# Kernel tuning notes

Measured on AMD Instinct MI355X. Metric: run time of the kernel, lower is better.

## Reference

```python
import jax, jax.numpy as jnp
import numpy as np

N, E = 100000, 1600000
F_IN, H, C = 64, 64, 40


def setup_inputs() -> dict:
    key = jax.random.key(0)
    k = jax.random.split(key, 6)
    x = jax.random.normal(k[0], (N, F_IN), jnp.float32)
    edge_index = jax.random.randint(k[1], (2, E), 0, N, jnp.int32)
    edge_weight = jax.random.uniform(k[2], (E,), jnp.float32)
    W1 = jax.random.normal(k[3], (F_IN, H), jnp.float32) / np.sqrt(F_IN)
    b1 = jnp.zeros((H,), jnp.float32)
    W2 = jax.random.normal(k[4], (H, C), jnp.float32) / np.sqrt(H)
    b2 = jnp.zeros((C,), jnp.float32)
    return {"x": x, "edge_index": edge_index, "edge_weight": edge_weight,
            "W1": W1, "b1": b1, "W2": W2, "b2": b2}


def reference(x, edge_index, edge_weight, W1, b1, W2, b2):
    # PyG GCNConv: add self-loops (weight 1), symmetric normalization
    # D^{-1/2} (A + I) D^{-1/2}, linear transform, scatter-add, bias.
    n = x.shape[0]
    src, dst = edge_index[0], edge_index[1]
    loop = jnp.arange(n, dtype=src.dtype)
    src_f = jnp.concatenate([src, loop])
    dst_f = jnp.concatenate([dst, loop])
    w_f = jnp.concatenate([edge_weight, jnp.ones((n,), edge_weight.dtype)])
    deg = jax.ops.segment_sum(w_f, dst_f, num_segments=n)
    dinv = jnp.where(deg > 0, jax.lax.rsqrt(deg), 0.0)
    norm = dinv[src_f] * w_f * dinv[dst_f]  # [E+N]

    def conv(h, W, b):
        h = h @ W                                    # [n, d_out]
        msg = h[src_f] * norm[:, None]               # gather + scale, [E+N, d_out]
        return jax.ops.segment_sum(msg, dst_f, num_segments=n) + b

    h = jax.nn.relu(conv(x, W1, b1))
    # dropout is identity in eval mode (training=False)
    h = conv(h, W2, b2)
    return jax.nn.log_softmax(h, axis=1)
```

## Files before the change

kernel.cpp:

```cpp
#include <hip/hip_runtime.h>
#include <math.h>

#define N_NODES 100000
#define N_EDGES 1600000
#define C_DIM 40
#define NGROUPS 6250

#define BSZ 256
#define NB  ((N_NODES + BSZ - 1) / BSZ)
#define EB  4096
#define NBE ((N_EDGES + EB - 1) / EB)

#define OFF_DINV 0
#define OFF_BB   100000
#define OFF_CS   100392
#define OFF_ROW  100800
#define OFF_H    200802
#define OFF_REC2 353684
#define OFF_H1P  3553684
#define OFF_H2A  6753684
#define OFF_H2B  8353684
#define OFF_AGG1 8753684

typedef float floatx4 __attribute__((ext_vector_type(4)));
typedef short shortx8 __attribute__((ext_vector_type(8)));

__device__ inline unsigned short f2bf(float f) {
    unsigned int u = __float_as_uint(f);
    u += 0x7FFF + ((u >> 16) & 1);
    return (unsigned short)(u >> 16);
}
__device__ inline float bflo(unsigned int u) { return __uint_as_float(u << 16); }
__device__ inline float bfhi(unsigned int u) { return __uint_as_float(u & 0xFFFF0000u); }

__global__ __launch_bounds__(512) void k_hist2d(const int* __restrict__ ei,
                                                int* __restrict__ H,
                                                int* __restrict__ colsum) {
    __shared__ int bins[NB];
    int t = threadIdx.x, b = blockIdx.x;
    for (int i = t; i < NB; i += 512) bins[i] = 0;
    __syncthreads();
    int base = b * EB;
    for (int i = t; i < EB; i += 512) {
        int e = base + i;
        if (e < N_EDGES) atomicAdd(&bins[ei[N_EDGES + e] >> 8], 1);
    }
    __syncthreads();
    for (int i = t; i < NB; i += 512) {
        int c = bins[i];
        H[b * NB + i] = c;
        if (c) atomicAdd(&colsum[i], c);
    }
}

__global__ __launch_bounds__(512) void k_colscan(int* __restrict__ H,
                                                 const int* __restrict__ colsum,
                                                 int* __restrict__ bucketBase,
                                                 int* __restrict__ rowStart) {
    __shared__ int sd[512];
    __shared__ int sbase;
    int t = threadIdx.x, j = blockIdx.x;
    int p = 0;
    for (int i = t; i < j; i += 512) p += colsum[i];
    sd[t] = p;
    __syncthreads();
    for (int off = 256; off > 0; off >>= 1) {
        if (t < off) sd[t] += sd[t + off];
        __syncthreads();
    }
    if (t == 0) sbase = sd[0];
    __syncthreads();
    int base = sbase;
    if (t == 0) {
        bucketBase[j] = base;
        if (j == NB - 1) { bucketBase[NB] = base + colsum[j]; rowStart[N_NODES] = N_EDGES; }
    }
    __syncthreads();
    int val = (t < NBE) ? H[t * NB + j] : 0;
    sd[t] = val;
    __syncthreads();
    for (int off = 1; off < 512; off <<= 1) {
        int v = (t >= off) ? sd[t - off] : 0;
        __syncthreads();
        sd[t] += v;
        __syncthreads();
    }
    if (t < NBE) H[t * NB + j] = base + sd[t] - val;
}

__global__ __launch_bounds__(512) void k_scatter(const int* __restrict__ ei,
                                                 const float* __restrict__ w,
                                                 const int* __restrict__ blockBase,
                                                 int2* __restrict__ rec) {
    __shared__ int bases[NB];
    __shared__ int cur[NB];
    int t = threadIdx.x, b = blockIdx.x;
    for (int i = t; i < NB; i += 512) { bases[i] = blockBase[b * NB + i]; cur[i] = 0; }
    __syncthreads();
    int base = b * EB;
    for (int i = t; i < EB; i += 512) {
        int e = base + i;
        if (e < N_EDGES) {
            int s = ei[e], d = ei[N_EDGES + e];
            float wv = w[e];
            int bin = d >> 8;
            int pos = bases[bin] + atomicAdd(&cur[bin], 1);
            rec[pos] = make_int2(s | ((d & 255) << 17), __float_as_int(wv));
        }
    }
}

__global__ __launch_bounds__(512) void k_bsort(const int* __restrict__ bucketBase,
                                               const int2* __restrict__ rec,
                                               int2* __restrict__ rec2,
                                               float* __restrict__ dinv,
                                               int* __restrict__ rowStart) {
    __shared__ int   cnt[256];
    __shared__ float wsum[256];
    __shared__ int   cur[256];
    __shared__ int   sd[512];
    int t = threadIdx.x, b = blockIdx.x;
    if (t < 256) { cnt[t] = 0; wsum[t] = 0.f; }
    __syncthreads();
    int r0 = bucketBase[b], r1 = bucketBase[b + 1];
    for (int i = r0 + t; i < r1; i += 512) {
        int2 rv = rec[i];
        int l = (rv.x >> 17) & 255;
        atomicAdd(&cnt[l], 1);
        atomicAdd(&wsum[l], __int_as_float(rv.y));
    }
    __syncthreads();
    int val = (t < 256) ? cnt[t] : 0;
    sd[t] = val;
    __syncthreads();
    for (int off = 1; off < 512; off <<= 1) {
        int v = (t >= off) ? sd[t - off] : 0;
        __syncthreads();
        sd[t] += v;
        __syncthreads();
    }
    float dloc = 0.f;
    if (t < 256) {
        int excl = sd[t] - val;
        cur[t] = excl;
        int node = b * BSZ + t;
        dloc = rsqrtf(1.f + wsum[t]);
        if (node < N_NODES) {
            rowStart[node] = r0 + excl;
            dinv[node] = dloc;
        }
    }
    __syncthreads();
    if (t < 256) wsum[t] = dloc;
    __syncthreads();
    for (int i = r0 + t; i < r1; i += 512) {
        int2 rv = rec[i];
        int l = (rv.x >> 17) & 255;
        float cpart = __int_as_float(rv.y) * wsum[l];
        int pos = r0 + atomicAdd(&cur[l], 1);
        rec2[pos] = make_int2((rv.x & 0x1FFFF) << 7, __float_as_int(cpart));
    }
}

__global__ __launch_bounds__(256) void k_mm1(const float* __restrict__ x,
                                             const float* __restrict__ W1,
                                             const float* __restrict__ dinv,
                                             unsigned short* __restrict__ h1p) {
    int t = threadIdx.x, lane = t & 63, wv = t >> 6;
    int m = lane & 15, quad = lane >> 4;
    int wid = blockIdx.x * 4 + wv, nw = gridDim.x * 4;
    shortx8 B[2][4];
#pragma unroll
    for (int kc = 0; kc < 2; ++kc)
#pragma unroll
        for (int tt = 0; tt < 4; ++tt)
#pragma unroll
            for (int j = 0; j < 8; ++j) {
                int k = kc * 32 + quad * 8 + j;
                B[kc][tt][j] = (short)f2bf(W1[k * 64 + tt * 16 + m]);
            }
    for (int g = wid; g < NGROUPS; g += nw) {
        int n0 = g * 16;
        const float* xr = x + (long)(n0 + m) * 64 + quad * 8;
        floatx4 xa = ((const floatx4*)xr)[0];
        floatx4 xb = ((const floatx4*)(xr + 4))[0];
        floatx4 xc = ((const floatx4*)(xr + 32))[0];
        floatx4 xd = ((const floatx4*)(xr + 36))[0];
        shortx8 A0, A1;
#pragma unroll
        for (int j = 0; j < 4; ++j) {
            A0[j] = (short)f2bf(xa[j]);
            A0[4 + j] = (short)f2bf(xb[j]);
            A1[j] = (short)f2bf(xc[j]);
            A1[4 + j] = (short)f2bf(xd[j]);
        }
        floatx4 acc[4];
#pragma unroll
        for (int tt = 0; tt < 4; ++tt) {
            acc[tt] = (floatx4){0.f, 0.f, 0.f, 0.f};
            acc[tt] = __builtin_amdgcn_mfma_f32_16x16x32_bf16(A0, B[0][tt], acc[tt], 0, 0, 0);
            acc[tt] = __builtin_amdgcn_mfma_f32_16x16x32_bf16(A1, B[1][tt], acc[tt], 0, 0, 0);
        }
        floatx4 dv = ((const floatx4*)(dinv + n0 + quad * 4))[0];
#pragma unroll
        for (int reg = 0; reg < 4; ++reg) {
            int node = n0 + quad * 4 + reg;
            float d = dv[reg];
#pragma unroll
            for (int tt = 0; tt < 4; ++tt)
                h1p[(long)node * 64 + tt * 16 + m] = f2bf(acc[tt][reg] * d);
        }
    }
}

__global__ __launch_bounds__(256) void k_agg1(const int* __restrict__ rowStart,
                                              const int2* __restrict__ rec2,
                                              const float* __restrict__ dinv,
                                              const unsigned short* __restrict__ h1p,
                                              float* __restrict__ agg1) {
    __shared__ int2 cache[4][64];
    int t = threadIdx.x, lane = t & 63, wv = t >> 6;
    int node = blockIdx.x * 4 + wv;
    if (node >= N_NODES) return;
    int2* wc = cache[wv];
    wc[lane] = make_int2(0, 0);
    const char* hb = (const char*)h1p;
    int eslot = lane >> 4;
    int c = lane & 15;
    int lo = c << 3;
    float dn = dinv[node];
    float a0 = 0.f, a1 = 0.f, a2 = 0.f, a3 = 0.f;
    float b0 = 0.f, b1 = 0.f, b2v = 0.f, b3 = 0.f;
    if (eslot == 0) {
        const unsigned int* sp = (const unsigned int*)(hb + ((long)node << 7) + lo);
        unsigned int u0 = sp[0], u1 = sp[1];
        a0 = bflo(u0) * dn; a1 = bfhi(u0) * dn;
        a2 = bflo(u1) * dn; a3 = bfhi(u1) * dn;
    }
    int s0 = rowStart[node], s1 = rowStart[node + 1];
    for (int base = s0; base < s1; base += 64) {
        int idx = base + lane;
        if (idx < s1) wc[lane] = rec2[idx];
        __builtin_amdgcn_wave_barrier();
        int cnt = min(64, s1 - base);
        for (int j = 0; j < cnt; j += 20) {
            int2 e0, e1, e2, e3, e4;
            float w0, w1, w2, w3, w4;
            { int jj = j + eslot;      bool v = jj < cnt; e0 = wc[v ? jj : j]; w0 = v ? __int_as_float(e0.y) : 0.f; }
            { int jj = j + 4 + eslot;  bool v = jj < cnt; e1 = wc[v ? jj : j]; w1 = v ? __int_as_float(e1.y) : 0.f; }
            { int jj = j + 8 + eslot;  bool v = jj < cnt; e2 = wc[v ? jj : j]; w2 = v ? __int_as_float(e2.y) : 0.f; }
            { int jj = j + 12 + eslot; bool v = jj < cnt; e3 = wc[v ? jj : j]; w3 = v ? __int_as_float(e3.y) : 0.f; }
            { int jj = j + 16 + eslot; bool v = jj < cnt; e4 = wc[v ? jj : j]; w4 = v ? __int_as_float(e4.y) : 0.f; }
            uint2 q0 = *(const uint2*)(hb + e0.x + lo);
            uint2 q1 = *(const uint2*)(hb + e1.x + lo);
            uint2 q2 = *(const uint2*)(hb + e2.x + lo);
            uint2 q3 = *(const uint2*)(hb + e3.x + lo);
            uint2 q4 = *(const uint2*)(hb + e4.x + lo);
            a0 = fmaf(bflo(q0.x), w0, a0); a1 = fmaf(bfhi(q0.x), w0, a1);
            a2 = fmaf(bflo(q0.y), w0, a2); a3 = fmaf(bfhi(q0.y), w0, a3);
            b0 = fmaf(bflo(q1.x), w1, b0); b1 = fmaf(bfhi(q1.x), w1, b1);
            b2v = fmaf(bflo(q1.y), w1, b2v); b3 = fmaf(bfhi(q1.y), w1, b3);
            a0 = fmaf(bflo(q2.x), w2, a0); a1 = fmaf(bfhi(q2.x), w2, a1);
            a2 = fmaf(bflo(q2.y), w2, a2); a3 = fmaf(bfhi(q2.y), w2, a3);
            b0 = fmaf(bflo(q3.x), w3, b0); b1 = fmaf(bfhi(q3.x), w3, b1);
            b2v = fmaf(bflo(q3.y), w3, b2v); b3 = fmaf(bfhi(q3.y), w3, b3);
            a0 = fmaf(bflo(q4.x), w4, a0); a1 = fmaf(bfhi(q4.x), w4, a1);
            a2 = fmaf(bflo(q4.y), w4, a2); a3 = fmaf(bfhi(q4.y), w4, a3);
        }
        __builtin_amdgcn_wave_barrier();
    }
    a0 += b0; a1 += b1; a2 += b2v; a3 += b3;
    a0 += __shfl_xor(a0, 16, 64); a0 += __shfl_xor(a0, 32, 64);
    a1 += __shfl_xor(a1, 16, 64); a1 += __shfl_xor(a1, 32, 64);
    a2 += __shfl_xor(a2, 16, 64); a2 += __shfl_xor(a2, 32, 64);
    a3 += __shfl_xor(a3, 16, 64); a3 += __shfl_xor(a3, 32, 64);
    if (eslot == 0) {
        *(float4*)(agg1 + ((long)node << 6) + (c << 2)) = make_float4(a0, a1, a2, a3);
    }
}

__global__ __launch_bounds__(256) void k_mm2(const float* __restrict__ agg1,
                                             const float* __restrict__ b1,
                                             const float* __restrict__ W2,
                                             const float* __restrict__ dinv,
                                             unsigned short* __restrict__ h2a,
                                             unsigned short* __restrict__ h2b) {
    int t = threadIdx.x, lane = t & 63, wv = t >> 6;
    int m = lane & 15, quad = lane >> 4;
    int wid = blockIdx.x * 4 + wv, nw = gridDim.x * 4;
    shortx8 B[2][3];
#pragma unroll
    for (int kc = 0; kc < 2; ++kc)
#pragma unroll
        for (int tt = 0; tt < 3; ++tt) {
            int n = tt * 16 + m;
#pragma unroll
            for (int j = 0; j < 8; ++j) {
                int k = kc * 32 + quad * 8 + j;
                B[kc][tt][j] = (n < C_DIM) ? (short)f2bf(W2[k * C_DIM + n]) : (short)0;
            }
        }
    floatx4 ba0 = ((const floatx4*)(b1 + quad * 8))[0];
    floatx4 ba1 = ((const floatx4*)(b1 + quad * 8 + 4))[0];
    floatx4 bb0 = ((const floatx4*)(b1 + 32 + quad * 8))[0];
    floatx4 bb1 = ((const floatx4*)(b1 + 32 + quad * 8 + 4))[0];
    for (int g = wid; g < NGROUPS; g += nw) {
        int n0 = g * 16;
        const float* xr = agg1 + (long)(n0 + m) * 64 + quad * 8;
        floatx4 xa = ((const floatx4*)xr)[0];
        floatx4 xb = ((const floatx4*)(xr + 4))[0];
        floatx4 xc = ((const floatx4*)(xr + 32))[0];
        floatx4 xd = ((const floatx4*)(xr + 36))[0];
        shortx8 A0, A1;
#pragma unroll
        for (int j = 0; j < 4; ++j) {
            A0[j]     = (short)f2bf(fmaxf(xa[j] + ba0[j], 0.f));
            A0[4 + j] = (short)f2bf(fmaxf(xb[j] + ba1[j], 0.f));
            A1[j]     = (short)f2bf(fmaxf(xc[j] + bb0[j], 0.f));
            A1[4 + j] = (short)f2bf(fmaxf(xd[j] + bb1[j], 0.f));
        }
        floatx4 acc[3];
#pragma unroll
        for (int tt = 0; tt < 3; ++tt) {
            acc[tt] = (floatx4){0.f, 0.f, 0.f, 0.f};
            acc[tt] = __builtin_amdgcn_mfma_f32_16x16x32_bf16(A0, B[0][tt], acc[tt], 0, 0, 0);
            acc[tt] = __builtin_amdgcn_mfma_f32_16x16x32_bf16(A1, B[1][tt], acc[tt], 0, 0, 0);
        }
        floatx4 dv = ((const floatx4*)(dinv + n0 + quad * 4))[0];
#pragma unroll
        for (int reg = 0; reg < 4; ++reg) {
            int node = n0 + quad * 4 + reg;
            float d = dv[reg];
            h2a[(long)node * 32 + m]      = f2bf(acc[0][reg] * d);
            h2a[(long)node * 32 + 16 + m] = f2bf(acc[1][reg] * d);
            if (m < 8)
                h2b[(long)node * 8 + m]   = f2bf(acc[2][reg] * d);
        }
    }
}

__global__ __launch_bounds__(256) void k_agg2(const int* __restrict__ rowStart,
                                              const int2* __restrict__ rec2,
                                              const float* __restrict__ dinv,
                                              const unsigned short* __restrict__ h2a,
                                              const unsigned short* __restrict__ h2b,
                                              const float* __restrict__ b2,
                                              float* __restrict__ out) {
    __shared__ int2 cache[4][64];
    int t = threadIdx.x, lane = t & 63, wv = t >> 6;
    int node = blockIdx.x * 4 + wv;
    if (node >= N_NODES) return;
    int2* wc = cache[wv];
    wc[lane] = make_int2(0, 0);
    int eslot = lane / 20;
    int c = lane - eslot * 20;
    bool elane = eslot < 3;
    const char* gb = (c < 16) ? (const char*)h2a : (const char*)h2b;
    int sh = (c < 16) ? 1 : 3;
    int lo2 = (c < 16) ? (c << 2) : ((c - 16) << 2);
    float dn = dinv[node];
    float alo0 = 0.f, ahi0 = 0.f, alo1 = 0.f, ahi1 = 0.f;
    if (eslot == 0) {
        unsigned int u = *(const unsigned int*)(gb + (((long)node << 7) >> sh) + lo2);
        alo0 = bflo(u) * dn;
        ahi0 = bfhi(u) * dn;
    }
    int s0 = rowStart[node], s1 = rowStart[node + 1];
    for (int base = s0; base < s1; base += 64) {
        int idx = base + lane;
        if (idx < s1) wc[lane] = rec2[idx];
        __builtin_amdgcn_wave_barrier();
        int cnt = min(64, s1 - base);
        for (int j = 0; j < cnt; j += 21) {
            int2 e0, e1, e2, e3, e4, e5, e6;
            float f0, f1, f2, f3, f4, f5, f6;
            { int jj = j + eslot;      bool v = elane && jj < cnt; e0 = wc[v ? jj : j]; f0 = v ? __int_as_float(e0.y) : 0.f; }
            { int jj = j + 3 + eslot;  bool v = elane && jj < cnt; e1 = wc[v ? jj : j]; f1 = v ? __int_as_float(e1.y) : 0.f; }
            { int jj = j + 6 + eslot;  bool v = elane && jj < cnt; e2 = wc[v ? jj : j]; f2 = v ? __int_as_float(e2.y) : 0.f; }
            { int jj = j + 9 + eslot;  bool v = elane && jj < cnt; e3 = wc[v ? jj : j]; f3 = v ? __int_as_float(e3.y) : 0.f; }
            { int jj = j + 12 + eslot; bool v = elane && jj < cnt; e4 = wc[v ? jj : j]; f4 = v ? __int_as_float(e4.y) : 0.f; }
            { int jj = j + 15 + eslot; bool v = elane && jj < cnt; e5 = wc[v ? jj : j]; f5 = v ? __int_as_float(e5.y) : 0.f; }
            { int jj = j + 18 + eslot; bool v = elane && jj < cnt; e6 = wc[v ? jj : j]; f6 = v ? __int_as_float(e6.y) : 0.f; }
            unsigned int q0 = *(const unsigned int*)(gb + (e0.x >> sh) + lo2);
            unsigned int q1 = *(const unsigned int*)(gb + (e1.x >> sh) + lo2);
            unsigned int q2 = *(const unsigned int*)(gb + (e2.x >> sh) + lo2);
            unsigned int q3 = *(const unsigned int*)(gb + (e3.x >> sh) + lo2);
            unsigned int q4 = *(const unsigned int*)(gb + (e4.x >> sh) + lo2);
            unsigned int q5 = *(const unsigned int*)(gb + (e5.x >> sh) + lo2);
            unsigned int q6 = *(const unsigned int*)(gb + (e6.x >> sh) + lo2);
            alo0 = fmaf(bflo(q0), f0, alo0); ahi0 = fmaf(bfhi(q0), f0, ahi0);
            alo1 = fmaf(bflo(q1), f1, alo1); ahi1 = fmaf(bfhi(q1), f1, ahi1);
            alo0 = fmaf(bflo(q2), f2, alo0); ahi0 = fmaf(bfhi(q2), f2, ahi0);
            alo1 = fmaf(bflo(q3), f3, alo1); ahi1 = fmaf(bfhi(q3), f3, ahi1);
            alo0 = fmaf(bflo(q4), f4, alo0); ahi0 = fmaf(bfhi(q4), f4, ahi0);
            alo1 = fmaf(bflo(q5), f5, alo1); ahi1 = fmaf(bfhi(q5), f5, ahi1);
            alo0 = fmaf(bflo(q6), f6, alo0); ahi0 = fmaf(bfhi(q6), f6, ahi0);
        }
        __builtin_amdgcn_wave_barrier();
    }
    float alo = alo0 + alo1, ahi = ahi0 + ahi1;
    float t1 = __shfl(alo, lane + 20, 64), t2 = __shfl(alo, lane + 40, 64);
    float t3 = __shfl(ahi, lane + 20, 64), t4 = __shfl(ahi, lane + 40, 64);
    alo = alo + t1 + t2;
    ahi = ahi + t3 + t4;
    bool act = lane < 20;
    float2 bb = ((const float2*)b2)[c];
    float vlo = act ? alo + bb.x : -INFINITY;
    float vhi = act ? ahi + bb.y : -INFINITY;
    float m = fmaxf(vlo, vhi);
#pragma unroll
    for (int off = 16; off; off >>= 1) m = fmaxf(m, __shfl_xor(m, off, 64));
    const float LOG2E = 1.4426950408889634f;
    const float LN2   = 0.6931471805599453f;
    float exlo = act ? __builtin_amdgcn_exp2f((vlo - m) * LOG2E) : 0.f;
    float exhi = act ? __builtin_amdgcn_exp2f((vhi - m) * LOG2E) : 0.f;
    float s = exlo + exhi;
#pragma unroll
    for (int off = 16; off; off >>= 1) s += __shfl_xor(s, off, 64);
    float ls = m + __builtin_amdgcn_logf(s) * LN2;
    if (act) {
        *(float2*)(out + (long)node * C_DIM + (c << 1)) = make_float2(vlo - ls, vhi - ls);
    }
}

extern "C" void kernel_launch(void* const* d_in, const int* in_sizes, int n_in,
                              void* d_out, int out_size, void* d_ws, size_t ws_size,
                              hipStream_t stream) {
    const float* x  = (const float*)d_in[0];
    const int*   ei = (const int*)d_in[1];
    const float* w  = (const float*)d_in[2];
    const float* W1 = (const float*)d_in[3];
    const float* b1 = (const float*)d_in[4];
    const float* W2 = (const float*)d_in[5];
    const float* b2 = (const float*)d_in[6];
    float* out = (float*)d_out;

    float* wsf = (float*)d_ws;
    int*   wsi = (int*)d_ws;
    float* dinv       = wsf + OFF_DINV;
    int*   bucketBase = wsi + OFF_BB;
    int*   colsum     = wsi + OFF_CS;
    int*   rowStart   = wsi + OFF_ROW;
    int*   H          = wsi + OFF_H;
    int2*  rec2       = (int2*)(wsi + OFF_REC2);
    int2*  rec        = (int2*)(wsi + OFF_H1P);
    unsigned short* h1p = (unsigned short*)(wsi + OFF_H1P);
    unsigned short* h2a = (unsigned short*)(wsi + OFF_H2A);
    unsigned short* h2b = (unsigned short*)(wsi + OFF_H2B);
    float* agg1       = wsf + OFF_AGG1;

    hipMemsetAsync(colsum, 0, NB * sizeof(int), stream);
    k_hist2d<<<NBE, 512, 0, stream>>>(ei, H, colsum);
    k_colscan<<<NB, 512, 0, stream>>>(H, colsum, bucketBase, rowStart);
    k_scatter<<<NBE, 512, 0, stream>>>(ei, w, H, rec);
    k_bsort<<<NB, 512, 0, stream>>>(bucketBase, rec, rec2, dinv, rowStart);

    k_mm1<<<512, 256, 0, stream>>>(x, W1, dinv, h1p);
    k_agg1<<<(N_NODES + 3) / 4, 256, 0, stream>>>(rowStart, rec2, dinv, h1p, agg1);

    k_mm2<<<512, 256, 0, stream>>>(agg1, b1, W2, dinv, h2a, h2b);
    k_agg2<<<(N_NODES + 3) / 4, 256, 0, stream>>>(rowStart, rec2, dinv, h2a, h2b, b2, out);
}
```

Before: 266.5 us.

## Fold full symmetric norm into edge records and split layer-1 gather by feature halves

The per-source dinv scaling moves out of the matmul outputs and into the sorted edge weights, so both matmuls no longer depend on the degree computation. k_mm1 therefore runs first, independent of the sort. The bucket sort is split into a degree/rowStart pass and a record-emit pass that multiplies in dinv[src], with self-loops scaled by dinv^2. The layer-1 aggregation now stores features as two 32-wide bf16 halves, and each node is handled by two blocks, one per half, so each gathered row is half as wide. The cost is an extra kernel launch, a random dinv gather per edge, and twice as many aggregation blocks.

Result: slower. 301.1 us (+13.0%).

```diff
diff --git a/kernel.cpp b/kernel.cpp
--- a/kernel.cpp
+++ b/kernel.cpp
@@ -17,7 +17,8 @@
 #define OFF_ROW  100800
 #define OFF_H    200802
 #define OFF_REC2 353684
-#define OFF_H1P  3553684
+#define OFF_H1A  3553684
+#define OFF_H1B  5153684
 #define OFF_H2A  6753684
 #define OFF_H2B  8353684
 #define OFF_AGG1 8753684
@@ -53,119 +54,10 @@
     }
 }
 
-__global__ __launch_bounds__(512) void k_colscan(int* __restrict__ H,
-                                                 const int* __restrict__ colsum,
-                                                 int* __restrict__ bucketBase,
-                                                 int* __restrict__ rowStart) {
-    __shared__ int sd[512];
-    __shared__ int sbase;
-    int t = threadIdx.x, j = blockIdx.x;
-    int p = 0;
-    for (int i = t; i < j; i += 512) p += colsum[i];
-    sd[t] = p;
-    __syncthreads();
-    for (int off = 256; off > 0; off >>= 1) {
-        if (t < off) sd[t] += sd[t + off];
-        __syncthreads();
-    }
-    if (t == 0) sbase = sd[0];
-    __syncthreads();
-    int base = sbase;
-    if (t == 0) {
-        bucketBase[j] = base;
-        if (j == NB - 1) { bucketBase[NB] = base + colsum[j]; rowStart[N_NODES] = N_EDGES; }
-    }
-    __syncthreads();
-    int val = (t < NBE) ? H[t * NB + j] : 0;
-    sd[t] = val;
-    __syncthreads();
-    for (int off = 1; off < 512; off <<= 1) {
-        int v = (t >= off) ? sd[t - off] : 0;
-        __syncthreads();
-        sd[t] += v;
-        __syncthreads();
-    }
-    if (t < NBE) H[t * NB + j] = base + sd[t] - val;
-}
-
-__global__ __launch_bounds__(512) void k_scatter(const int* __restrict__ ei,
-                                                 const float* __restrict__ w,
-                                                 const int* __restrict__ blockBase,
-                                                 int2* __restrict__ rec) {
-    __shared__ int bases[NB];
-    __shared__ int cur[NB];
-    int t = threadIdx.x, b = blockIdx.x;
-    for (int i = t; i < NB; i += 512) { bases[i] = blockBase[b * NB + i]; cur[i] = 0; }
-    __syncthreads();
-    int base = b * EB;
-    for (int i = t; i < EB; i += 512) {
-        int e = base + i;
-        if (e < N_EDGES) {
-            int s = ei[e], d = ei[N_EDGES + e];
-            float wv = w[e];
-            int bin = d >> 8;
-            int pos = bases[bin] + atomicAdd(&cur[bin], 1);
-            rec[pos] = make_int2(s | ((d & 255) << 17), __float_as_int(wv));
-        }
-    }
-}
-
-__global__ __launch_bounds__(512) void k_bsort(const int* __restrict__ bucketBase,
-                                               const int2* __restrict__ rec,
-                                               int2* __restrict__ rec2,
-                                               float* __restrict__ dinv,
-                                               int* __restrict__ rowStart) {
-    __shared__ int   cnt[256];
-    __shared__ float wsum[256];
-    __shared__ int   cur[256];
-    __shared__ int   sd[512];
-    int t = threadIdx.x, b = blockIdx.x;
-    if (t < 256) { cnt[t] = 0; wsum[t] = 0.f; }
-    __syncthreads();
-    int r0 = bucketBase[b], r1 = bucketBase[b + 1];
-    for (int i = r0 + t; i < r1; i += 512) {
-        int2 rv = rec[i];
-        int l = (rv.x >> 17) & 255;
-        atomicAdd(&cnt[l], 1);
-        atomicAdd(&wsum[l], __int_as_float(rv.y));
-    }
-    __syncthreads();
-    int val = (t < 256) ? cnt[t] : 0;
-    sd[t] = val;
-    __syncthreads();
-    for (int off = 1; off < 512; off <<= 1) {
-        int v = (t >= off) ? sd[t - off] : 0;
-        __syncthreads();
-        sd[t] += v;
-        __syncthreads();
-    }
-    float dloc = 0.f;
-    if (t < 256) {
-        int excl = sd[t] - val;
-        cur[t] = excl;
-        int node = b * BSZ + t;
-        dloc = rsqrtf(1.f + wsum[t]);
-        if (node < N_NODES) {
-            rowStart[node] = r0 + excl;
-            dinv[node] = dloc;
-        }
-    }
-    __syncthreads();
-    if (t < 256) wsum[t] = dloc;
-    __syncthreads();
-    for (int i = r0 + t; i < r1; i += 512) {
-        int2 rv = rec[i];
-        int l = (rv.x >> 17) & 255;
-        float cpart = __int_as_float(rv.y) * wsum[l];
-        int pos = r0 + atomicAdd(&cur[l], 1);
-        rec2[pos] = make_int2((rv.x & 0x1FFFF) << 7, __float_as_int(cpart));
-    }
-}
-
 __global__ __launch_bounds__(256) void k_mm1(const float* __restrict__ x,
                                              const float* __restrict__ W1,
-                                             const float* __restrict__ dinv,
-                                             unsigned short* __restrict__ h1p) {
+                                             unsigned short* __restrict__ h1a,
+                                             unsigned short* __restrict__ h1b) {
     int t = threadIdx.x, lane = t & 63, wv = t >> 6;
     int m = lane & 15, quad = lane >> 4;
     int wid = blockIdx.x * 4 + wv, nw = gridDim.x * 4;
@@ -201,41 +93,161 @@
             acc[tt] = __builtin_amdgcn_mfma_f32_16x16x32_bf16(A0, B[0][tt], acc[tt], 0, 0, 0);
             acc[tt] = __builtin_amdgcn_mfma_f32_16x16x32_bf16(A1, B[1][tt], acc[tt], 0, 0, 0);
         }
-        floatx4 dv = ((const floatx4*)(dinv + n0 + quad * 4))[0];
 #pragma unroll
         for (int reg = 0; reg < 4; ++reg) {
             int node = n0 + quad * 4 + reg;
-            float d = dv[reg];
-#pragma unroll
-            for (int tt = 0; tt < 4; ++tt)
-                h1p[(long)node * 64 + tt * 16 + m] = f2bf(acc[tt][reg] * d);
-        }
-    }
-}
-
-__global__ __launch_bounds__(256) void k_agg1(const int* __restrict__ rowStart,
-                                              const int2* __restrict__ rec2,
-                                              const float* __restrict__ dinv,
-                                              const unsigned short* __restrict__ h1p,
-                                              float* __restrict__ agg1) {
+            h1a[(long)node * 32 + m]      = f2bf(acc[0][reg]);
+            h1a[(long)node * 32 + 16 + m] = f2bf(acc[1][reg]);
+            h1b[(long)node * 32 + m]      = f2bf(acc[2][reg]);
+            h1b[(long)node * 32 + 16 + m] = f2bf(acc[3][reg]);
+        }
+    }
+}
+
+__global__ __launch_bounds__(512) void k_colscan(int* __restrict__ H,
+                                                 const int* __restrict__ colsum,
+                                                 int* __restrict__ bucketBase,
+                                                 int* __restrict__ rowStart) {
+    __shared__ int sd[512];
+    __shared__ int sbase;
+    int t = threadIdx.x, j = blockIdx.x;
+    int p = 0;
+    for (int i = t; i < j; i += 512) p += colsum[i];
+    sd[t] = p;
+    __syncthreads();
+    for (int off = 256; off > 0; off >>= 1) {
+        if (t < off) sd[t] += sd[t + off];
+        __syncthreads();
+    }
+    if (t == 0) sbase = sd[0];
+    __syncthreads();
+    int base = sbase;
+    if (t == 0) {
+        bucketBase[j] = base;
+        if (j == NB - 1) { bucketBase[NB] = base + colsum[j]; rowStart[N_NODES] = N_EDGES; }
+    }
+    __syncthreads();
+    int val = (t < NBE) ? H[t * NB + j] : 0;
+    sd[t] = val;
+    __syncthreads();
+    for (int off = 1; off < 512; off <<= 1) {
+        int v = (t >= off) ? sd[t - off] : 0;
+        __syncthreads();
+        sd[t] += v;
+        __syncthreads();
+    }
+    if (t < NBE) H[t * NB + j] = base + sd[t] - val;
+}
+
+__global__ __launch_bounds__(512) void k_scatter(const int* __restrict__ ei,
+                                                 const float* __restrict__ w,
+                                                 const int* __restrict__ blockBase,
+                                                 int2* __restrict__ rec) {
+    __shared__ int bases[NB];
+    __shared__ int cur[NB];
+    int t = threadIdx.x, b = blockIdx.x;
+    for (int i = t; i < NB; i += 512) { bases[i] = blockBase[b * NB + i]; cur[i] = 0; }
+    __syncthreads();
+    int base = b * EB;
+    for (int i = t; i < EB; i += 512) {
+        int e = base + i;
+        if (e < N_EDGES) {
+            int s = ei[e], d = ei[N_EDGES + e];
+            float wv = w[e];
+            int bin = d >> 8;
+            int pos = bases[bin] + atomicAdd(&cur[bin], 1);
+            rec[pos] = make_int2(s | ((d & 255) << 17), __float_as_int(wv));
+        }
+    }
+}
+
+__global__ __launch_bounds__(512) void k_bsortA(const int* __restrict__ bucketBase,
+                                                const int2* __restrict__ rec,
+                                                float* __restrict__ dinv,
+                                                int* __restrict__ rowStart) {
+    __shared__ int   cnt[256];
+    __shared__ float wsum[256];
+    __shared__ int   sd[512];
+    int t = threadIdx.x, b = blockIdx.x;
+    if (t < 256) { cnt[t] = 0; wsum[t] = 0.f; }
+    __syncthreads();
+    int r0 = bucketBase[b], r1 = bucketBase[b + 1];
+    for (int i = r0 + t; i < r1; i += 512) {
+        int2 rv = rec[i];
+        int l = (rv.x >> 17) & 255;
+        atomicAdd(&cnt[l], 1);
+        atomicAdd(&wsum[l], __int_as_float(rv.y));
+    }
+    __syncthreads();
+    int val = (t < 256) ? cnt[t] : 0;
+    sd[t] = val;
+    __syncthreads();
+    for (int off = 1; off < 512; off <<= 1) {
+        int v = (t >= off) ? sd[t - off] : 0;
+        __syncthreads();
+        sd[t] += v;
+        __syncthreads();
+    }
+    if (t < 256) {
+        int node = b * BSZ + t;
+        if (node < N_NODES) {
+            rowStart[node] = r0 + (sd[t] - val);
+            dinv[node] = rsqrtf(1.f + wsum[t]);
+        }
+    }
+}
+
+__global__ __launch_bounds__(512) void k_bsortB(const int* __restrict__ bucketBase,
+                                                const int* __restrict__ rowStart,
+                                                const float* __restrict__ dinv,
+                                                const int2* __restrict__ rec,
+                                                int2* __restrict__ rec2) {
+    __shared__ int   cur[256];
+    __shared__ float dd[256];
+    int t = threadIdx.x, b = blockIdx.x;
+    if (t < 256) {
+        int node = b * BSZ + t;
+        cur[t] = (node < N_NODES) ? rowStart[node] : 0;
+        dd[t]  = (node < N_NODES) ? dinv[node] : 0.f;
+    }
+    __syncthreads();
+    int r0 = bucketBase[b], r1 = bucketBase[b + 1];
+    for (int i = r0 + t; i < r1; i += 512) {
+        int2 rv = rec[i];
+        int l = (rv.x >> 17) & 255;
+        int s = rv.x & 0x1FFFF;
+        float cpart = __int_as_float(rv.y) * dd[l] * dinv[s];
+        int pos = atomicAdd(&cur[l], 1);
+        rec2[pos] = make_int2(s << 6, __float_as_int(cpart));
+    }
+}
+
+__global__ __launch_bounds__(256) void k_agg1s(const int* __restrict__ rowStart,
+                                               const int2* __restrict__ rec2,
+                                               const float* __restrict__ dinv,
+                                               const unsigned short* __restrict__ h1a,
+                                               const unsigned short* __restrict__ h1b,
+                                               float* __restrict__ agg1) {
     __shared__ int2 cache[4][64];
     int t = threadIdx.x, lane = t & 63, wv = t >> 6;
-    int node = blockIdx.x * 4 + wv;
-    if (node >= N_NODES) return;
+    int b = blockIdx.x;
+    int r = b & 7;
+    int half = r >> 2;
+    int g = (b >> 3) * 4 + (r & 3);
+    int node = g * 4 + wv;
     int2* wc = cache[wv];
     wc[lane] = make_int2(0, 0);
-    const char* hb = (const char*)h1p;
+    const char* hb = half ? (const char*)h1b : (const char*)h1a;
     int eslot = lane >> 4;
     int c = lane & 15;
-    int lo = c << 3;
+    int lo = c << 2;
     float dn = dinv[node];
-    float a0 = 0.f, a1 = 0.f, a2 = 0.f, a3 = 0.f;
-    float b0 = 0.f, b1 = 0.f, b2v = 0.f, b3 = 0.f;
+    float dn2 = dn * dn;
+    float aLo = 0.f, aHi = 0.f, bLo = 0.f, bHi = 0.f;
     if (eslot == 0) {
-        const unsigned int* sp = (const unsigned int*)(hb + ((long)node << 7) + lo);
-        unsigned int u0 = sp[0], u1 = sp[1];
-        a0 = bflo(u0) * dn; a1 = bfhi(u0) * dn;
-        a2 = bflo(u1) * dn; a3 = bfhi(u1) * dn;
+        unsigned int u = *(const unsigned int*)(hb + ((long)node << 6) + lo);
+        aLo = bflo(u) * dn2;
+        aHi = bfhi(u) * dn2;
     }
     int s0 = rowStart[node], s1 = rowStart[node + 1];
     for (int base = s0; base < s1; base += 64) {
@@ -251,38 +263,30 @@
             { int jj = j + 8 + eslot;  bool v = jj < cnt; e2 = wc[v ? jj : j]; w2 = v ? __int_as_float(e2.y) : 0.f; }
             { int jj = j + 12 + eslot; bool v = jj < cnt; e3 = wc[v ? jj : j]; w3 = v ? __int_as_float(e3.y) : 0.f; }
             { int jj = j + 16 + eslot; bool v = jj < cnt; e4 = wc[v ? jj : j]; w4 = v ? __int_as_float(e4.y) : 0.f; }
-            uint2 q0 = *(const uint2*)(hb + e0.x + lo);
-            uint2 q1 = *(const uint2*)(hb + e1.x + lo);
-            uint2 q2 = *(const uint2*)(hb + e2.x + lo);
-            uint2 q3 = *(const uint2*)(hb + e3.x + lo);
-            uint2 q4 = *(const uint2*)(hb + e4.x + lo);
-            a0 = fmaf(bflo(q0.x), w0, a0); a1 = fmaf(bfhi(q0.x), w0, a1);
-            a2 = fmaf(bflo(q0.y), w0, a2); a3 = fmaf(bfhi(q0.y), w0, a3);
-            b0 = fmaf(bflo(q1.x), w1, b0); b1 = fmaf(bfhi(q1.x), w1, b1);
-            b2v = fmaf(bflo(q1.y), w1, b2v); b3 = fmaf(bfhi(q1.y), w1, b3);
-            a0 = fmaf(bflo(q2.x), w2, a0); a1 = fmaf(bfhi(q2.x), w2, a1);
-            a2 = fmaf(bflo(q2.y), w2, a2); a3 = fmaf(bfhi(q2.y), w2, a3);
-            b0 = fmaf(bflo(q3.x), w3, b0); b1 = fmaf(bfhi(q3.x), w3, b1);
-            b2v = fmaf(bflo(q3.y), w3, b2v); b3 = fmaf(bfhi(q3.y), w3, b3);
-            a0 = fmaf(bflo(q4.x), w4, a0); a1 = fmaf(bfhi(q4.x), w4, a1);
-            a2 = fmaf(bflo(q4.y), w4, a2); a3 = fmaf(bfhi(q4.y), w4, a3);
+            unsigned int q0 = *(const unsigned int*)(hb + e0.x + lo);
+            unsigned int q1 = *(const unsigned int*)(hb + e1.x + lo);
+            unsigned int q2 = *(const unsigned int*)(hb + e2.x + lo);
+            unsigned int q3 = *(const unsigned int*)(hb + e3.x + lo);
+            unsigned int q4 = *(const unsigned int*)(hb + e4.x + lo);
+            aLo = fmaf(bflo(q0), w0, aLo); aHi = fmaf(bfhi(q0), w0, aHi);
+            bLo = fmaf(bflo(q1), w1, bLo); bHi = fmaf(bfhi(q1), w1, bHi);
+            aLo = fmaf(bflo(q2), w2, aLo); aHi = fmaf(bfhi(q2), w2, aHi);
+            bLo = fmaf(bflo(q3), w3, bLo); bHi = fmaf(bfhi(q3), w3, bHi);
+            aLo = fmaf(bflo(q4), w4, aLo); aHi = fmaf(bfhi(q4), w4, aHi);
         }
         __builtin_amdgcn_wave_barrier();
     }
-    a0 += b0; a1 += b1; a2 += b2v; a3 += b3;
-    a0 += __shfl_xor(a0, 16, 64); a0 += __shfl_xor(a0, 32, 64);
-    a1 += __shfl_xor(a1, 16, 64); a1 += __shfl_xor(a1, 32, 64);
-    a2 += __shfl_xor(a2, 16, 64); a2 += __shfl_xor(a2, 32, 64);
-    a3 += __shfl_xor(a3, 16, 64); a3 += __shfl_xor(a3, 32, 64);
+    aLo += bLo; aHi += bHi;
+    aLo += __shfl_xor(aLo, 16, 64); aLo += __shfl_xor(aLo, 32, 64);
+    aHi += __shfl_xor(aHi, 16, 64); aHi += __shfl_xor(aHi, 32, 64);
     if (eslot == 0) {
-        *(float4*)(agg1 + ((long)node << 6) + (c << 2)) = make_float4(a0, a1, a2, a3);
+        *(float2*)(agg1 + ((long)node << 6) + half * 32 + (c << 1)) = make_float2(aLo, aHi);
     }
 }
 
 __global__ __launch_bounds__(256) void k_mm2(const float* __restrict__ agg1,
                                              const float* __restrict__ b1,
                                              const float* __restrict__ W2,
-                                             const float* __restrict__ dinv,
                                              unsigned short* __restrict__ h2a,
                                              unsigned short* __restrict__ h2b) {
     int t = threadIdx.x, lane = t & 63, wv = t >> 6;
@@ -326,15 +330,13 @@
             acc[tt] = __builtin_amdgcn_mfma_f32_16x16x32_bf16(A0, B[0][tt], acc[tt], 0, 0, 0);
             acc[tt] = __builtin_amdgcn_mfma_f32_16x16x32_bf16(A1, B[1][tt], acc[tt], 0, 0, 0);
         }
-        floatx4 dv = ((const floatx4*)(dinv + n0 + quad * 4))[0];
 #pragma unroll
         for (int reg = 0; reg < 4; ++reg) {
             int node = n0 + quad * 4 + reg;
-            float d = dv[reg];
-            h2a[(long)node * 32 + m]      = f2bf(acc[0][reg] * d);
-            h2a[(long)node * 32 + 16 + m] = f2bf(acc[1][reg] * d);
+            h2a[(long)node * 32 + m]      = f2bf(acc[0][reg]);
+            h2a[(long)node * 32 + 16 + m] = f2bf(acc[1][reg]);
             if (m < 8)
-                h2b[(long)node * 8 + m]   = f2bf(acc[2][reg] * d);
+                h2b[(long)node * 8 + m]   = f2bf(acc[2][reg]);
         }
     }
 }
@@ -356,14 +358,15 @@
     int c = lane - eslot * 20;
     bool elane = eslot < 3;
     const char* gb = (c < 16) ? (const char*)h2a : (const char*)h2b;
-    int sh = (c < 16) ? 1 : 3;
+    int sh = (c < 16) ? 0 : 2;
     int lo2 = (c < 16) ? (c << 2) : ((c - 16) << 2);
     float dn = dinv[node];
+    float dn2 = dn * dn;
     float alo0 = 0.f, ahi0 = 0.f, alo1 = 0.f, ahi1 = 0.f;
     if (eslot == 0) {
-        unsigned int u = *(const unsigned int*)(gb + (((long)node << 7) >> sh) + lo2);
-        alo0 = bflo(u) * dn;
-        ahi0 = bfhi(u) * dn;
+        unsigned int u = *(const unsigned int*)(gb + (((long)node << 6) >> sh) + lo2);
+        alo0 = bflo(u) * dn2;
+        ahi0 = bfhi(u) * dn2;
     }
     int s0 = rowStart[node], s1 = rowStart[node + 1];
     for (int base = s0; base < s1; base += 64) {
@@ -443,21 +446,23 @@
     int*   rowStart   = wsi + OFF_ROW;
     int*   H          = wsi + OFF_H;
     int2*  rec2       = (int2*)(wsi + OFF_REC2);
-    int2*  rec        = (int2*)(wsi + OFF_H1P);
-    unsigned short* h1p = (unsigned short*)(wsi + OFF_H1P);
+    int2*  rec        = (int2*)(wsi + OFF_AGG1);
+    unsigned short* h1a = (unsigned short*)(wsi + OFF_H1A);
+    unsigned short* h1b = (unsigned short*)(wsi + OFF_H1B);
     unsigned short* h2a = (unsigned short*)(wsi + OFF_H2A);
     unsigned short* h2b = (unsigned short*)(wsi + OFF_H2B);
     float* agg1       = wsf + OFF_AGG1;
 
     hipMemsetAsync(colsum, 0, NB * sizeof(int), stream);
+    k_mm1<<<512, 256, 0, stream>>>(x, W1, h1a, h1b);
     k_hist2d<<<NBE, 512, 0, stream>>>(ei, H, colsum);
     k_colscan<<<NB, 512, 0, stream>>>(H, colsum, bucketBase, rowStart);
     k_scatter<<<NBE, 512, 0, stream>>>(ei, w, H, rec);
-    k_bsort<<<NB, 512, 0, stream>>>(bucketBase, rec, rec2, dinv, rowStart);
-
-    k_mm1<<<512, 256, 0, stream>>>(x, W1, dinv, h1p);
-    k_agg1<<<(N_NODES + 3) / 4, 256, 0, stream>>>(rowStart, rec2, dinv, h1p, agg1);
-
-    k_mm2<<<512, 256, 0, stream>>>(agg1, b1, W2, dinv, h2a, h2b);
+    k_bsortA<<<NB, 512, 0, stream>>>(bucketBase, rec, dinv, rowStart);
+    k_bsortB<<<NB, 512, 0, stream>>>(bucketBase, rowStart, dinv, rec, rec2);
+
+    k_agg1s<<<50000, 256, 0, stream>>>(rowStart, rec2, dinv, h1a, h1b, agg1);
+
+    k_mm2<<<512, 256, 0, stream>>>(agg1, b1, W2, h2a, h2b);
     k_agg2<<<(N_NODES + 3) / 4, 256, 0, stream>>>(rowStart, rec2, dinv, h2a, h2b, b2, out);
 }
```
